# Kernel optimization log

Hardware: AMD Instinct MI355X
Metric: run time of the kernel (lower is better)

## Reference

```python
import jax, jax.numpy as jnp
import numpy as np

N_NODES = 20000
N_EDGES = 160000
N_CONFIG = 1000
OP_SIZE = 120
OP_FEATURE = 140
CONFIG_FEATURE = 24
HID = 256
EMB = 128


def _mynorm(x, axis):
    # InstanceNorm1d (affine=False): biased var, eps=1e-5, normalized over `axis`
    m = jnp.mean(x, axis=axis, keepdims=True)
    v = jnp.var(x, axis=axis, keepdims=True)
    return (x - m) / jnp.sqrt(v + 1e-5)


def _gelu(x):
    return jax.nn.gelu(x, approximate=False)


def _segment_softmax(e, seg, num):
    m = jax.ops.segment_max(e, seg, num_segments=num)
    ex = jnp.exp(e - m[seg])
    s = jax.ops.segment_sum(ex, seg, num_segments=num)
    return ex / (s[seg] + 1e-16)


def setup_inputs() -> dict:
    key = jax.random.key(0)
    ks = jax.random.split(key, 24)
    d = {}
    d['node_feat'] = jax.random.normal(ks[0], (N_NODES, OP_FEATURE), jnp.float32)
    d['config_feat'] = jax.random.normal(ks[1], (N_CONFIG, CONFIG_FEATURE), jnp.float32)
    d['node_feat_mean'] = jax.random.normal(ks[2], (OP_FEATURE,), jnp.float32)
    d['node_feat_std'] = jax.random.uniform(ks[3], (OP_FEATURE,), jnp.float32)
    d['config_feat_mean'] = jax.random.normal(ks[4], (CONFIG_FEATURE,), jnp.float32)
    d['config_feat_std'] = jax.random.uniform(ks[5], (CONFIG_FEATURE,), jnp.float32)
    d['embed_table'] = jax.random.normal(ks[6], (OP_SIZE, EMB), jnp.float32)
    d['early_W1'] = jax.random.normal(ks[7], (EMB + OP_FEATURE, HID), jnp.float32) * 0.05
    d['early_W2'] = jax.random.normal(ks[8], (HID, HID), jnp.float32) * 0.05
    d['gat_Wl'] = jax.random.normal(ks[9], (4, HID, HID), jnp.float32) * 0.05
    d['gat_bl'] = jax.random.normal(ks[10], (4, HID), jnp.float32) * 0.05
    d['gat_Wr'] = jax.random.normal(ks[11], (4, HID, HID), jnp.float32) * 0.05
    d['gat_br'] = jax.random.normal(ks[12], (4, HID), jnp.float32) * 0.05
    d['gat_att'] = jax.random.normal(ks[13], (4, HID), jnp.float32) * 0.05
    d['gat_bias'] = jax.random.normal(ks[14], (4, HID), jnp.float32) * 0.05
    d['late_W1'] = jax.random.normal(ks[15], (HID + CONFIG_FEATURE, HID), jnp.float32) * 0.05
    d['late_W2'] = jax.random.normal(ks[16], (HID, HID // 2), jnp.float32) * 0.05
    d['pred_W'] = jax.random.normal(ks[17], (HID // 2, 1), jnp.float32) * 0.05
    d['pred_b'] = jax.random.normal(ks[18], (1,), jnp.float32) * 0.05
    d['node_opcode'] = jax.random.randint(ks[19], (N_NODES,), 0, OP_SIZE, jnp.int64)
    d['edge_index'] = jax.random.randint(ks[20], (2, N_EDGES), 0, N_NODES, jnp.int64)
    return d


def reference(node_feat, config_feat, node_feat_mean, node_feat_std,
              config_feat_mean, config_feat_std, embed_table,
              early_W1, early_W2, gat_Wl, gat_bl, gat_Wr, gat_br,
              gat_att, gat_bias, late_W1, late_W2, pred_W, pred_b,
              node_opcode, edge_index):
    N = node_feat.shape[0]
    # embedding with max_norm=1: renormalize looked-up rows to L2 norm <= 1
    emb = embed_table[node_opcode]
    nrm = jnp.sqrt(jnp.sum(emb * emb, axis=-1, keepdims=True))
    emb = emb * jnp.minimum(1.0, 1.0 / (nrm + 1e-7))
    feat = (node_feat - node_feat_mean) / (node_feat_std + 1e-4)
    x = jnp.concatenate([emb, feat], axis=-1)  # [N, 268]
    # early MLP (norm over node axis per channel)
    x = _gelu(_mynorm(x @ early_W1, 0))
    x = _gelu(_mynorm(x @ early_W2, 0))
    # add self loops (PyG GATv2Conv default)
    loop = jnp.arange(N, dtype=edge_index.dtype)
    src = jnp.concatenate([edge_index[0], loop])  # message source j
    dst = jnp.concatenate([edge_index[1], loop])  # message target i
    for i in range(4):
        xl = x @ gat_Wl[i] + gat_bl[i]
        xr = x @ gat_Wr[i] + gat_br[i]
        h = xl[src] + xr[dst]                      # [E+N, HID]
        e = jax.nn.leaky_relu(h, 0.2) @ gat_att[i]  # [E+N]
        alpha = _segment_softmax(e, dst, N)
        out = jax.ops.segment_sum(alpha[:, None] * xl[src], dst, num_segments=N)
        out = out + gat_bias[i]
        x = _gelu(_mynorm(out, 0))
    pool = jnp.mean(x, axis=0) + jnp.max(x, axis=0)  # [HID]
    cf = (config_feat - config_feat_mean) / (config_feat_std + 1e-4)
    C = cf.shape[0]
    x_late = jnp.concatenate([cf, jnp.broadcast_to(pool, (C, pool.shape[0]))], axis=1)
    h = _gelu(_mynorm(x_late @ late_W1, 0))  # 2D MyNorm1d normalizes over batch axis
    h = _gelu(_mynorm(h @ late_W2, 0))
    runtime = (h @ pred_W + pred_b)[:, 0]
    return runtime
```

## Files before the change

### kernel.cpp

```cpp
#include <hip/hip_runtime.h>
#include <math.h>

#define N_NODES 20000
#define N_EDGES 160000
#define N_CFG   1000
#define OP_FEAT 140
#define CFG_FEAT 24
#define HID     256
#define EMB     128
#define E_TOT   (N_EDGES + N_NODES)
#define K288    288
#define MPAD    20096
#define NW      512

typedef __attribute__((ext_vector_type(8))) short short8v;
typedef __attribute__((ext_vector_type(4))) float f32x4;

__device__ __forceinline__ short f2bf(float f) {
  unsigned u = __float_as_uint(f);
  unsigned r = (u + 0x7FFFu + ((u >> 16) & 1u)) >> 16;
  return (short)r;
}
__device__ __forceinline__ float bf2f(short s) {
  return __uint_as_float(((unsigned)(unsigned short)s) << 16);
}
__device__ __forceinline__ float gelu_f(float x) {
  return 0.5f * x * (1.0f + erff(x * 0.70710678118654752f));
}

#define GLOAD_LDS(gptr, lptr) __builtin_amdgcn_global_load_lds( \
    (const __attribute__((address_space(1))) void*)(gptr),      \
    (__attribute__((address_space(3))) void*)(lptr), 16, 0, 0)

__global__ void prep_weights(
    const float* __restrict__ eW1, const float* __restrict__ eW2,
    const float* __restrict__ lW1, const float* __restrict__ lW2,
    const float* __restrict__ Wl, const float* __restrict__ Wr,
    const float* __restrict__ bl, const float* __restrict__ br,
    short* __restrict__ W1t, short* __restrict__ W2t,
    short* __restrict__ lW1t, short* __restrict__ lW2t,
    short* __restrict__ Wlrt, float* __restrict__ blr)
{
  int i = blockIdx.x * 256 + threadIdx.x;
  const int s1 = HID * K288;
  const int s2 = HID * HID;
  const int s3 = HID * K288;
  const int s4 = 128 * HID;
  const int s5 = 4 * NW * HID;
  const int s6 = 4 * NW;
  if (i < s1) { int n = i / K288, k = i % K288;
    W1t[i] = (k < EMB + OP_FEAT) ? f2bf(eW1[(size_t)k * HID + n]) : (short)0; return; }
  i -= s1;
  if (i < s2) { int n = i >> 8, k = i & 255;
    W2t[i] = f2bf(eW2[(size_t)k * HID + n]); return; }
  i -= s2;
  if (i < s3) { int n = i / K288, k = i % K288;
    lW1t[i] = (k < CFG_FEAT + HID) ? f2bf(lW1[(size_t)k * HID + n]) : (short)0; return; }
  i -= s3;
  if (i < s4) { int n = i >> 8, k = i & 255;
    lW2t[i] = f2bf(lW2[(size_t)k * 128 + n]); return; }
  i -= s4;
  if (i < s5) { int l = i >> 17, rem = i & 131071, n = rem >> 8, k = rem & 255;
    float v = (n < HID) ? Wl[(size_t)l * HID * HID + (size_t)k * HID + n]
                        : Wr[(size_t)l * HID * HID + (size_t)k * HID + (n - HID)];
    Wlrt[i] = f2bf(v); return; }
  i -= s5;
  if (i < s6) { int l = i >> 9, j = i & 511;
    blr[i] = (j < HID) ? bl[l * HID + j] : br[l * HID + j - HID]; }
}

__global__ __launch_bounds__(256) void prep_kernel(
    const float* __restrict__ node_feat, const float* __restrict__ nf_mean,
    const float* __restrict__ nf_std, const float* __restrict__ emb_table,
    const int* __restrict__ opcode, short* __restrict__ x268b)
{
  int wave = threadIdx.x >> 6;
  int lane = threadIdx.x & 63;
  int row = blockIdx.x * 4 + wave;
  if (row >= N_NODES) return;
  int op = opcode[row];
  float t0 = emb_table[op * EMB + lane];
  float t1 = emb_table[op * EMB + 64 + lane];
  float ss = t0 * t0 + t1 * t1;
  #pragma unroll
  for (int off = 32; off; off >>= 1) ss += __shfl_xor(ss, off);
  float sc = fminf(1.0f, 1.0f / (sqrtf(ss) + 1e-7f));
  short* dst = x268b + (size_t)row * K288;
  dst[lane] = f2bf(t0 * sc);
  dst[64 + lane] = f2bf(t1 * sc);
  for (int k = lane; k < OP_FEAT; k += 64)
    dst[EMB + k] = f2bf((node_feat[(size_t)row * OP_FEAT + k] - nf_mean[k]) / (nf_std[k] + 1e-4f));
  if (lane < K288 - EMB - OP_FEAT) dst[EMB + OP_FEAT + lane] = 0;
}

__global__ __launch_bounds__(256) void gemm_mfma(
    const short* __restrict__ A, const short* __restrict__ Wt,
    const float* __restrict__ bias, float* __restrict__ C,
    float* __restrict__ stats, int M, int N, int Kpad)
{
  __shared__ __align__(16) short As[4][128][8];
  __shared__ __align__(16) short Bs[4][128][8];
  int tid = threadIdx.x;
  int wave = tid >> 6, lane = tid & 63;
  int bm = blockIdx.x * 128, bn = blockIdx.y * 128;
  int wr = (wave >> 1) * 64, wc = (wave & 1) * 64;
  int g = lane >> 4, r16 = lane & 15;
  f32x4 acc[4][4] = {};

  for (int k0 = 0; k0 < Kpad; k0 += 32) {
    #pragma unroll
    for (int s2 = 0; s2 < 2; s2++) {
      int s = wave * 2 + s2;
      int sg = s >> 1, r0 = (s & 1) * 64;
      GLOAD_LDS(A  + (size_t)(bm + r0 + lane) * Kpad + k0 + sg * 8, &As[sg][r0][0]);
      GLOAD_LDS(Wt + (size_t)(bn + r0 + lane) * Kpad + k0 + sg * 8, &Bs[sg][r0][0]);
    }
    __syncthreads();
    short8v af[4], bfv[4];
    #pragma unroll
    for (int mi = 0; mi < 4; mi++)
      af[mi] = *(const short8v*)&As[g][wr + mi * 16 + r16][0];
    #pragma unroll
    for (int ni = 0; ni < 4; ni++)
      bfv[ni] = *(const short8v*)&Bs[g][wc + ni * 16 + r16][0];
    #pragma unroll
    for (int mi = 0; mi < 4; mi++)
      #pragma unroll
      for (int ni = 0; ni < 4; ni++)
        acc[mi][ni] = __builtin_amdgcn_mfma_f32_16x16x32_bf16(af[mi], bfv[ni], acc[mi][ni], 0, 0, 0);
    __syncthreads();
  }

  int rg = lane >> 4;
  #pragma unroll
  for (int ni = 0; ni < 4; ni++) {
    int gc = bn + wc + ni * 16 + r16;
    float bv = bias ? bias[gc] : 0.f;
    float s = 0.f, sq = 0.f;
    #pragma unroll
    for (int mi = 0; mi < 4; mi++) {
      #pragma unroll
      for (int r = 0; r < 4; r++) {
        int gr = bm + wr + mi * 16 + rg * 4 + r;
        if (gr < M) {
          float v = acc[mi][ni][r] + bv;
          C[(size_t)gr * N + gc] = v;
          s += v; sq += v * v;
        }
      }
    }
    if (stats) {
      s  += __shfl_xor(s, 16);  sq += __shfl_xor(sq, 16);
      s  += __shfl_xor(s, 32);  sq += __shfl_xor(sq, 32);
      if (rg == 0) { atomicAdd(&stats[gc], s); atomicAdd(&stats[N + gc], sq); }
    }
  }
}

__global__ void colstats(const float* __restrict__ X, int M, int C,
                         float* __restrict__ stats)
{
  int c = threadIdx.x;
  int r0 = blockIdx.x * 64;
  int r1 = min(r0 + 64, M);
  float s = 0.f, sq = 0.f;
  for (int r = r0; r < r1; r++) {
    float v = X[(size_t)r * C + c];
    s += v; sq += v * v;
  }
  atomicAdd(&stats[c], s);
  atomicAdd(&stats[C + c], sq);
}

__global__ void norm_gelu(const float* __restrict__ X, short* __restrict__ Yb,
                          int M, int C, const float* __restrict__ stats)
{
  int i = blockIdx.x * blockDim.x + threadIdx.x;
  if (i >= M * C) return;
  int c = i % C;
  float invM = 1.0f / (float)M;
  float mean = stats[c] * invM;
  float var = stats[C + c] * invM - mean * mean;
  float y = gelu_f((X[i] - mean) * rsqrtf(var + 1e-5f));
  Yb[i] = f2bf(y);
}

__global__ void edge_count(const int* __restrict__ ei, int* __restrict__ counts) {
  int e = blockIdx.x * blockDim.x + threadIdx.x;
  if (e >= E_TOT) return;
  int dst = (e < N_EDGES) ? ei[N_EDGES + e] : (e - N_EDGES);
  atomicAdd(&counts[dst], 1);
}

__global__ __launch_bounds__(1024) void scan_kernel(const int* __restrict__ counts,
                                                    int* __restrict__ indptr)
{
  __shared__ int sh[1024];
  int t = threadIdx.x;
  const int chunk = (N_NODES + 1023) / 1024;
  int start = t * chunk, end = min(start + chunk, N_NODES);
  int sum = 0;
  for (int i = start; i < end; i++) sum += counts[i];
  sh[t] = sum;
  __syncthreads();
  for (int off = 1; off < 1024; off <<= 1) {
    int v = (t >= off) ? sh[t - off] : 0;
    __syncthreads();
    sh[t] += v;
    __syncthreads();
  }
  int run = (t > 0) ? sh[t - 1] : 0;
  for (int i = start; i < end; i++) { indptr[i] = run; run += counts[i]; }
  if (t == 1023) indptr[N_NODES] = run;
}

__global__ void edge_fill(const int* __restrict__ ei, const int* __restrict__ indptr,
                          int* __restrict__ cursor, int* __restrict__ col)
{
  int e = blockIdx.x * blockDim.x + threadIdx.x;
  if (e >= E_TOT) return;
  int src, dst;
  if (e < N_EDGES) { src = ei[e]; dst = ei[N_EDGES + e]; }
  else             { src = dst = e - N_EDGES; }
  int pos = indptr[dst] + atomicAdd(&cursor[dst], 1);
  col[pos] = src;
}

__global__ __launch_bounds__(256) void gat_agg(
    const float* __restrict__ xlr,
    const int* __restrict__ indptr, const int* __restrict__ col,
    const float* __restrict__ att, const float* __restrict__ bias,
    float* __restrict__ out)
{
  int wave = threadIdx.x >> 6, lane = threadIdx.x & 63;
  int node = blockIdx.x * 4 + wave;
  if (node >= N_NODES) return;
  float attc[4], xri[4], o[4] = {0, 0, 0, 0};
  #pragma unroll
  for (int k = 0; k < 4; k++) {
    attc[k] = att[lane + 64 * k];
    xri[k] = xlr[(size_t)node * NW + HID + lane + 64 * k];
  }
  float m = -INFINITY, s = 0.f;
  int e0 = indptr[node], e1 = indptr[node + 1];
  for (int e = e0; e < e1; e++) {
    int j = col[e];
    float xlj[4], p = 0.f;
    #pragma unroll
    for (int k = 0; k < 4; k++) {
      xlj[k] = xlr[(size_t)j * NW + lane + 64 * k];
      float h = xlj[k] + xri[k];
      float lr = h > 0.f ? h : 0.2f * h;
      p += lr * attc[k];
    }
    #pragma unroll
    for (int off = 32; off; off >>= 1) p += __shfl_xor(p, off);
    float mn = fmaxf(m, p);
    float scale = __expf(m - mn);
    float w = __expf(p - mn);
    s = s * scale + w;
    #pragma unroll
    for (int k = 0; k < 4; k++) o[k] = o[k] * scale + w * xlj[k];
    m = mn;
  }
  float inv = 1.0f / (s + 1e-16f);
  #pragma unroll
  for (int k = 0; k < 4; k++)
    out[(size_t)node * HID + lane + 64 * k] = o[k] * inv + bias[lane + 64 * k];
}

__device__ __forceinline__ unsigned fenc(float f) {
  unsigned b = __float_as_uint(f);
  return (b & 0x80000000u) ? ~b : (b | 0x80000000u);
}
__device__ __forceinline__ float fdec(unsigned u) {
  unsigned b = (u & 0x80000000u) ? (u & 0x7FFFFFFFu) : ~u;
  return __uint_as_float(b);
}

__global__ void pool_reduce(const short* __restrict__ Xb, float* __restrict__ psum,
                            unsigned* __restrict__ pmax)
{
  int c = threadIdx.x;
  int r0 = blockIdx.x * 64, r1 = min(r0 + 64, N_NODES);
  float s = 0.f, mx = -INFINITY;
  for (int r = r0; r < r1; r++) {
    float v = bf2f(Xb[(size_t)r * HID + c]);
    s += v; mx = fmaxf(mx, v);
  }
  atomicAdd(&psum[c], s);
  atomicMax(&pmax[c], fenc(mx));
}

__global__ void build_xlate(const float* __restrict__ cfg, const float* __restrict__ cmean,
                            const float* __restrict__ cstd, const float* __restrict__ psum,
                            const unsigned* __restrict__ pmax, short* __restrict__ xlateb)
{
  int i = blockIdx.x * blockDim.x + threadIdx.x;
  if (i >= N_CFG * K288) return;
  int r = i / K288, c = i % K288;
  float v;
  if (c < CFG_FEAT) v = (cfg[r * CFG_FEAT + c] - cmean[c]) / (cstd[c] + 1e-4f);
  else if (c < CFG_FEAT + HID) {
    int p = c - CFG_FEAT;
    v = psum[p] * (1.0f / N_NODES) + fdec(pmax[p]);
  } else v = 0.f;
  xlateb[i] = f2bf(v);
}

__global__ __launch_bounds__(64) void pred_kernel(
    const float* __restrict__ h2, const float* __restrict__ stats,
    const float* __restrict__ W, const float* __restrict__ b,
    float* __restrict__ out)
{
  int r = blockIdx.x, lane = threadIdx.x;
  const float invM = 1.0f / (float)N_CFG;
  float v = 0.f;
  #pragma unroll
  for (int t = 0; t < 2; t++) {
    int c = lane + 64 * t;
    float mean = stats[c] * invM;
    float var = stats[128 + c] * invM - mean * mean;
    float y = gelu_f((h2[(size_t)r * 128 + c] - mean) * rsqrtf(var + 1e-5f));
    v += y * W[c];
  }
  #pragma unroll
  for (int off = 32; off; off >>= 1) v += __shfl_xor(v, off);
  if (lane == 0) out[r] = v + b[0];
}

extern "C" void kernel_launch(void* const* d_in, const int* in_sizes, int n_in,
                              void* d_out, int out_size, void* d_ws, size_t ws_size,
                              hipStream_t stream)
{
  const float* node_feat   = (const float*)d_in[0];
  const float* config_feat = (const float*)d_in[1];
  const float* nf_mean     = (const float*)d_in[2];
  const float* nf_std      = (const float*)d_in[3];
  const float* cf_mean     = (const float*)d_in[4];
  const float* cf_std      = (const float*)d_in[5];
  const float* emb_table   = (const float*)d_in[6];
  const float* early_W1    = (const float*)d_in[7];
  const float* early_W2    = (const float*)d_in[8];
  const float* gat_Wl      = (const float*)d_in[9];
  const float* gat_bl      = (const float*)d_in[10];
  const float* gat_Wr      = (const float*)d_in[11];
  const float* gat_br      = (const float*)d_in[12];
  const float* gat_att     = (const float*)d_in[13];
  const float* gat_bias    = (const float*)d_in[14];
  const float* late_W1     = (const float*)d_in[15];
  const float* late_W2     = (const float*)d_in[16];
  const float* pred_W      = (const float*)d_in[17];
  const float* pred_b      = (const float*)d_in[18];
  const int*   node_opcode = (const int*)d_in[19];
  const int*   edge_index  = (const int*)d_in[20];
  float* out = (float*)d_out;
  (void)in_sizes; (void)n_in; (void)out_size; (void)ws_size;

  char* ws = (char*)d_ws;
  size_t off = 0;
  auto alloc = [&](size_t bytes) -> void* {
    void* p = ws + off;
    off += (bytes + 255) & ~255ull;
    return p;
  };
  short* x268b = (short*)alloc((size_t)MPAD * K288 * 2);
  float* bufB  = (float*)alloc((size_t)N_NODES * HID * 4);
  short* bufAb = (short*)alloc((size_t)MPAD * HID * 2);
  float* xlr   = (float*)alloc((size_t)N_NODES * NW * 4);
  int* indptr  = (int*)alloc((N_NODES + 1) * 4);
  int* colidx  = (int*)alloc((size_t)E_TOT * 4);
  short* xlateb = (short*)alloc((size_t)1024 * K288 * 2);
  float* h1    = (float*)alloc((size_t)N_CFG * HID * 4);
  short* h1b   = (short*)alloc((size_t)1024 * HID * 2);
  float* h2    = (float*)alloc((size_t)N_CFG * 128 * 4);
  short* W1t   = (short*)alloc((size_t)HID * K288 * 2);
  short* W2t   = (short*)alloc((size_t)HID * HID * 2);
  short* Wlrt  = (short*)alloc((size_t)4 * NW * HID * 2);
  float* blr   = (float*)alloc(4 * NW * 4);
  short* lW1t  = (short*)alloc((size_t)HID * K288 * 2);
  short* lW2t  = (short*)alloc((size_t)128 * HID * 2);

  float* zbase = (float*)alloc((8 * 1024 + 512 + 2 * N_NODES) * 4);
  float* stats8 = zbase;
  float* psum   = zbase + 8192;
  unsigned* pmax = (unsigned*)(zbase + 8192 + 256);
  int* counts   = (int*)(zbase + 8192 + 512);
  int* cursor   = counts + N_NODES;
  const size_t zbytes = (8 * 1024 + 512 + 2 * N_NODES) * 4;
  auto slot = [&](int s) { return stats8 + s * 1024; };

  auto run_gemm = [&](const short* A, const short* Wt, const float* bias, float* C,
                      float* stats, int M, int N, int Kpad) {
    dim3 grid((M + 127) / 128, N / 128);
    hipLaunchKernelGGL(gemm_mfma, grid, dim3(256), 0, stream, A, Wt, bias, C, stats, M, N, Kpad);
  };

  hipMemsetAsync(zbase, 0, zbytes, stream);

  {
    int total = HID * K288 + HID * HID + HID * K288 + 128 * HID + 4 * NW * HID + 4 * NW;
    hipLaunchKernelGGL(prep_weights, dim3((total + 255) / 256), dim3(256), 0, stream,
                       early_W1, early_W2, late_W1, late_W2, gat_Wl, gat_Wr, gat_bl, gat_br,
                       W1t, W2t, lW1t, lW2t, Wlrt, blr);
  }

  hipLaunchKernelGGL(edge_count, dim3((E_TOT + 255) / 256), dim3(256), 0, stream,
                     edge_index, counts);
  hipLaunchKernelGGL(scan_kernel, dim3(1), dim3(1024), 0, stream, counts, indptr);
  hipLaunchKernelGGL(edge_fill, dim3((E_TOT + 255) / 256), dim3(256), 0, stream,
                     edge_index, indptr, cursor, colidx);

  hipLaunchKernelGGL(prep_kernel, dim3((N_NODES + 3) / 4), dim3(256), 0, stream,
                     node_feat, nf_mean, nf_std, emb_table, node_opcode, x268b);
  run_gemm(x268b, W1t, nullptr, bufB, slot(0), N_NODES, HID, K288);
  hipLaunchKernelGGL(norm_gelu, dim3((N_NODES * HID + 255) / 256), dim3(256), 0, stream,
                     bufB, bufAb, N_NODES, HID, slot(0));
  run_gemm(bufAb, W2t, nullptr, bufB, slot(1), N_NODES, HID, HID);
  hipLaunchKernelGGL(norm_gelu, dim3((N_NODES * HID + 255) / 256), dim3(256), 0, stream,
                     bufB, bufAb, N_NODES, HID, slot(1));

  for (int l = 0; l < 4; l++) {
    run_gemm(bufAb, Wlrt + (size_t)l * NW * HID, blr + l * NW, xlr, nullptr, N_NODES, NW, HID);
    hipLaunchKernelGGL(gat_agg, dim3((N_NODES + 3) / 4), dim3(256), 0, stream,
                       xlr, indptr, colidx, gat_att + l * HID, gat_bias + l * HID, bufB);
    hipLaunchKernelGGL(colstats, dim3((N_NODES + 63) / 64), dim3(HID), 0, stream,
                       bufB, N_NODES, HID, slot(2 + l));
    hipLaunchKernelGGL(norm_gelu, dim3((N_NODES * HID + 255) / 256), dim3(256), 0, stream,
                       bufB, bufAb, N_NODES, HID, slot(2 + l));
  }

  hipLaunchKernelGGL(pool_reduce, dim3((N_NODES + 63) / 64), dim3(HID), 0, stream,
                     bufAb, psum, pmax);

  hipLaunchKernelGGL(build_xlate, dim3((N_CFG * K288 + 255) / 256), dim3(256), 0, stream,
                     config_feat, cf_mean, cf_std, psum, pmax, xlateb);
  run_gemm(xlateb, lW1t, nullptr, h1, slot(6), N_CFG, HID, K288);
  hipLaunchKernelGGL(norm_gelu, dim3((N_CFG * HID + 255) / 256), dim3(256), 0, stream,
                     h1, h1b, N_CFG, HID, slot(6));
  run_gemm(h1b, lW2t, nullptr, h2, slot(7), N_CFG, 128, HID);
  hipLaunchKernelGGL(pred_kernel, dim3(N_CFG), dim3(64), 0, stream,
                     h2, slot(7), pred_W, pred_b, out);
}
```

Before: 601.1 us.

## Store GAT projections in bf16, double-buffer GEMM tiles, vectorize norm and aggregation

The xl/xr projection GEMM now writes bf16 instead of fp32, which halves the bytes read by the gather-heavy GAT aggregation. Aggregation loads four contiguous channels per lane as one vector. The MFMA GEMM gains a two-stage LDS double buffer so the next K tile is loaded while the current one is computed, and it drops one barrier per iteration. norm_gelu processes four elements per thread with vector loads and stores. The bf16 projections lose precision in the attention logits and messages, and the lane-to-channel mapping changes.

```diff
diff --git a/kernel.cpp b/kernel.cpp
--- a/kernel.cpp
+++ b/kernel.cpp
@@ -96,39 +96,48 @@
 __global__ __launch_bounds__(256) void gemm_mfma(
     const short* __restrict__ A, const short* __restrict__ Wt,
     const float* __restrict__ bias, float* __restrict__ C,
-    float* __restrict__ stats, int M, int N, int Kpad)
-{
-  __shared__ __align__(16) short As[4][128][8];
-  __shared__ __align__(16) short Bs[4][128][8];
+    short* __restrict__ Cb, float* __restrict__ stats,
+    int M, int N, int Kpad)
+{
+  __shared__ __align__(16) short As[2][4][128][8];
+  __shared__ __align__(16) short Bs[2][4][128][8];
   int tid = threadIdx.x;
   int wave = tid >> 6, lane = tid & 63;
   int bm = blockIdx.x * 128, bn = blockIdx.y * 128;
   int wr = (wave >> 1) * 64, wc = (wave & 1) * 64;
   int g = lane >> 4, r16 = lane & 15;
   f32x4 acc[4][4] = {};
-
-  for (int k0 = 0; k0 < Kpad; k0 += 32) {
+  int nt = Kpad >> 5;
+
+  int sA = wave * 2;
+  auto STAGE = [&](int t, int b) {
+    int k0 = t * 32;
     #pragma unroll
     for (int s2 = 0; s2 < 2; s2++) {
-      int s = wave * 2 + s2;
+      int s = sA + s2;
       int sg = s >> 1, r0 = (s & 1) * 64;
-      GLOAD_LDS(A  + (size_t)(bm + r0 + lane) * Kpad + k0 + sg * 8, &As[sg][r0][0]);
-      GLOAD_LDS(Wt + (size_t)(bn + r0 + lane) * Kpad + k0 + sg * 8, &Bs[sg][r0][0]);
+      GLOAD_LDS(A  + (size_t)(bm + r0 + lane) * Kpad + k0 + sg * 8, &As[b][sg][r0][0]);
+      GLOAD_LDS(Wt + (size_t)(bn + r0 + lane) * Kpad + k0 + sg * 8, &Bs[b][sg][r0][0]);
     }
+  };
+
+  STAGE(0, 0);
+  for (int t = 0; t < nt; t++) {
+    int b = t & 1;
     __syncthreads();
+    if (t + 1 < nt) STAGE(t + 1, b ^ 1);
     short8v af[4], bfv[4];
     #pragma unroll
     for (int mi = 0; mi < 4; mi++)
-      af[mi] = *(const short8v*)&As[g][wr + mi * 16 + r16][0];
+      af[mi] = *(const short8v*)&As[b][g][wr + mi * 16 + r16][0];
     #pragma unroll
     for (int ni = 0; ni < 4; ni++)
-      bfv[ni] = *(const short8v*)&Bs[g][wc + ni * 16 + r16][0];
+      bfv[ni] = *(const short8v*)&Bs[b][g][wc + ni * 16 + r16][0];
     #pragma unroll
     for (int mi = 0; mi < 4; mi++)
       #pragma unroll
       for (int ni = 0; ni < 4; ni++)
         acc[mi][ni] = __builtin_amdgcn_mfma_f32_16x16x32_bf16(af[mi], bfv[ni], acc[mi][ni], 0, 0, 0);
-    __syncthreads();
   }
 
   int rg = lane >> 4;
@@ -144,7 +153,8 @@
         int gr = bm + wr + mi * 16 + rg * 4 + r;
         if (gr < M) {
           float v = acc[mi][ni][r] + bv;
-          C[(size_t)gr * N + gc] = v;
+          if (C)  C[(size_t)gr * N + gc] = v;
+          if (Cb) Cb[(size_t)gr * N + gc] = f2bf(v);
           s += v; sq += v * v;
         }
       }
@@ -175,14 +185,21 @@
 __global__ void norm_gelu(const float* __restrict__ X, short* __restrict__ Yb,
                           int M, int C, const float* __restrict__ stats)
 {
-  int i = blockIdx.x * blockDim.x + threadIdx.x;
-  if (i >= M * C) return;
-  int c = i % C;
+  int i4 = blockIdx.x * blockDim.x + threadIdx.x;
+  int idx = i4 * 4;
+  if (idx >= M * C) return;
+  int c = idx & (C - 1);
   float invM = 1.0f / (float)M;
-  float mean = stats[c] * invM;
-  float var = stats[C + c] * invM - mean * mean;
-  float y = gelu_f((X[i] - mean) * rsqrtf(var + 1e-5f));
-  Yb[i] = f2bf(y);
+  f32x4 x = *(const f32x4*)(X + idx);
+  short4 y;
+  #pragma unroll
+  for (int j = 0; j < 4; j++) {
+    float mean = stats[c + j] * invM;
+    float var = stats[C + c + j] * invM - mean * mean;
+    float v = gelu_f((x[j] - mean) * rsqrtf(var + 1e-5f));
+    ((short*)&y)[j] = f2bf(v);
+  }
+  *(short4*)(Yb + idx) = y;
 }
 
 __global__ void edge_count(const int* __restrict__ ei, int* __restrict__ counts) {
@@ -227,7 +244,7 @@
 }
 
 __global__ __launch_bounds__(256) void gat_agg(
-    const float* __restrict__ xlr,
+    const short* __restrict__ xlr,
     const int* __restrict__ indptr, const int* __restrict__ col,
     const float* __restrict__ att, const float* __restrict__ bias,
     float* __restrict__ out)
@@ -236,19 +253,23 @@
   int node = blockIdx.x * 4 + wave;
   if (node >= N_NODES) return;
   float attc[4], xri[4], o[4] = {0, 0, 0, 0};
-  #pragma unroll
-  for (int k = 0; k < 4; k++) {
-    attc[k] = att[lane + 64 * k];
-    xri[k] = xlr[(size_t)node * NW + HID + lane + 64 * k];
+  {
+    short4 xr4 = *(const short4*)(xlr + (size_t)node * NW + HID + lane * 4);
+    #pragma unroll
+    for (int k = 0; k < 4; k++) {
+      attc[k] = att[lane * 4 + k];
+      xri[k] = bf2f(((short*)&xr4)[k]);
+    }
   }
   float m = -INFINITY, s = 0.f;
   int e0 = indptr[node], e1 = indptr[node + 1];
   for (int e = e0; e < e1; e++) {
     int j = col[e];
+    short4 xl4 = *(const short4*)(xlr + (size_t)j * NW + lane * 4);
     float xlj[4], p = 0.f;
     #pragma unroll
     for (int k = 0; k < 4; k++) {
-      xlj[k] = xlr[(size_t)j * NW + lane + 64 * k];
+      xlj[k] = bf2f(((short*)&xl4)[k]);
       float h = xlj[k] + xri[k];
       float lr = h > 0.f ? h : 0.2f * h;
       p += lr * attc[k];
@@ -264,9 +285,10 @@
     m = mn;
   }
   float inv = 1.0f / (s + 1e-16f);
-  #pragma unroll
-  for (int k = 0; k < 4; k++)
-    out[(size_t)node * HID + lane + 64 * k] = o[k] * inv + bias[lane + 64 * k];
+  f32x4 ov;
+  #pragma unroll
+  for (int k = 0; k < 4; k++) ov[k] = o[k] * inv + bias[lane * 4 + k];
+  *(f32x4*)(out + (size_t)node * HID + lane * 4) = ov;
 }
 
 __device__ __forceinline__ unsigned fenc(float f) {
@@ -367,7 +389,7 @@
   short* x268b = (short*)alloc((size_t)MPAD * K288 * 2);
   float* bufB  = (float*)alloc((size_t)N_NODES * HID * 4);
   short* bufAb = (short*)alloc((size_t)MPAD * HID * 2);
-  float* xlr   = (float*)alloc((size_t)N_NODES * NW * 4);
+  short* xlr   = (short*)alloc((size_t)N_NODES * NW * 2);
   int* indptr  = (int*)alloc((N_NODES + 1) * 4);
   int* colidx  = (int*)alloc((size_t)E_TOT * 4);
   short* xlateb = (short*)alloc((size_t)1024 * K288 * 2);
@@ -391,9 +413,10 @@
   auto slot = [&](int s) { return stats8 + s * 1024; };
 
   auto run_gemm = [&](const short* A, const short* Wt, const float* bias, float* C,
-                      float* stats, int M, int N, int Kpad) {
+                      short* Cb, float* stats, int M, int N, int Kpad) {
     dim3 grid((M + 127) / 128, N / 128);
-    hipLaunchKernelGGL(gemm_mfma, grid, dim3(256), 0, stream, A, Wt, bias, C, stats, M, N, Kpad);
+    hipLaunchKernelGGL(gemm_mfma, grid, dim3(256), 0, stream, A, Wt, bias, C, Cb, stats,
+                       M, N, Kpad);
   };
 
   hipMemsetAsync(zbase, 0, zbytes, stream);
@@ -413,20 +436,21 @@
 
   hipLaunchKernelGGL(prep_kernel, dim3((N_NODES + 3) / 4), dim3(256), 0, stream,
                      node_feat, nf_mean, nf_std, emb_table, node_opcode, x268b);
-  run_gemm(x268b, W1t, nullptr, bufB, slot(0), N_NODES, HID, K288);
-  hipLaunchKernelGGL(norm_gelu, dim3((N_NODES * HID + 255) / 256), dim3(256), 0, stream,
+  run_gemm(x268b, W1t, nullptr, bufB, nullptr, slot(0), N_NODES, HID, K288);
+  hipLaunchKernelGGL(norm_gelu, dim3((N_NODES * HID / 4 + 255) / 256), dim3(256), 0, stream,
                      bufB, bufAb, N_NODES, HID, slot(0));
-  run_gemm(bufAb, W2t, nullptr, bufB, slot(1), N_NODES, HID, HID);
-  hipLaunchKernelGGL(norm_gelu, dim3((N_NODES * HID + 255) / 256), dim3(256), 0, stream,
+  run_gemm(bufAb, W2t, nullptr, bufB, nullptr, slot(1), N_NODES, HID, HID);
+  hipLaunchKernelGGL(norm_gelu, dim3((N_NODES * HID / 4 + 255) / 256), dim3(256), 0, stream,
                      bufB, bufAb, N_NODES, HID, slot(1));
 
   for (int l = 0; l < 4; l++) {
-    run_gemm(bufAb, Wlrt + (size_t)l * NW * HID, blr + l * NW, xlr, nullptr, N_NODES, NW, HID);
+    run_gemm(bufAb, Wlrt + (size_t)l * NW * HID, blr + l * NW, nullptr, xlr, nullptr,
+             N_NODES, NW, HID);
     hipLaunchKernelGGL(gat_agg, dim3((N_NODES + 3) / 4), dim3(256), 0, stream,
                        xlr, indptr, colidx, gat_att + l * HID, gat_bias + l * HID, bufB);
     hipLaunchKernelGGL(colstats, dim3((N_NODES + 63) / 64), dim3(HID), 0, stream,
                        bufB, N_NODES, HID, slot(2 + l));
-    hipLaunchKernelGGL(norm_gelu, dim3((N_NODES * HID + 255) / 256), dim3(256), 0, stream,
+    hipLaunchKernelGGL(norm_gelu, dim3((N_NODES * HID / 4 + 255) / 256), dim3(256), 0, stream,
                        bufB, bufAb, N_NODES, HID, slot(2 + l));
   }
 
@@ -435,10 +459,10 @@
 
   hipLaunchKernelGGL(build_xlate, dim3((N_CFG * K288 + 255) / 256), dim3(256), 0, stream,
                      config_feat, cf_mean, cf_std, psum, pmax, xlateb);
-  run_gemm(xlateb, lW1t, nullptr, h1, slot(6), N_CFG, HID, K288);
-  hipLaunchKernelGGL(norm_gelu, dim3((N_CFG * HID + 255) / 256), dim3(256), 0, stream,
+  run_gemm(xlateb, lW1t, nullptr, h1, nullptr, slot(6), N_CFG, HID, K288);
+  hipLaunchKernelGGL(norm_gelu, dim3((N_CFG * HID / 4 + 255) / 256), dim3(256), 0, stream,
                      h1, h1b, N_CFG, HID, slot(6));
-  run_gemm(h1b, lW2t, nullptr, h2, slot(7), N_CFG, 128, HID);
+  run_gemm(h1b, lW2t, nullptr, h2, nullptr, slot(7), N_CFG, 128, HID);
   hipLaunchKernelGGL(pred_kernel, dim3(N_CFG), dim3(64), 0, stream,
                      h2, slot(7), pred_W, pred_b, out);
 }
```

Measured after the change: 605.7 us. About the same (+0.8%).
